# Kernel optimization log

Hardware: AMD Instinct MI355X
Metric: run time of the kernel (lower is better)

The kernel has to match this reference:

```python
import jax, jax.numpy as jnp
import numpy as np

EPS = 1e-5

def _layernorm(x, w, b):
    # x: [B, L, C]; WithBias_LayerNorm over last dim (biased variance)
    mu = jnp.mean(x, axis=-1, keepdims=True)
    var = jnp.mean((x - mu) ** 2, axis=-1, keepdims=True)
    return (x - mu) / jnp.sqrt(var + EPS) * w + b

def _selective_scan(x, x_proj_w, dt_w, A_logs, Ds):
    # x: [B, D, L]  (D = ssm d_inner = 192, N = d_state = 16, R = dt_rank = 6)
    Bsz, D, L = x.shape
    N = A_logs.shape[1]
    R = dt_w.shape[1]
    x_dbl = jnp.einsum('bdl,rd->blr', x, x_proj_w)            # [B, L, R+2N]
    dts_r = x_dbl[..., :R]
    Bs = x_dbl[..., R:R + N]                                   # [B, L, N]
    Cs = x_dbl[..., R + N:]                                    # [B, L, N]
    dts = jax.nn.softplus(jnp.einsum('blr,dr->bld', dts_r, dt_w))  # [B, L, D]
    As = -jnp.exp(A_logs.astype(jnp.float32))                  # [D, N]
    dt_A = jnp.exp(jnp.einsum('bld,dn->bldn', dts, As))        # [B, L, D, N]
    dt_B_x = jnp.einsum('bld,bln,bdl->bldn', dts, Bs, x)       # [B, L, D, N]

    def step(u, inp):
        a, bx, c = inp                                         # [B,D,N],[B,D,N],[B,N]
        u = a * u + bx
        y = jnp.einsum('bdn,bn->bd', u, c)
        return u, y

    u0 = jnp.zeros((Bsz, D, N), dtype=jnp.float32)
    _, ys = jax.lax.scan(step, u0, (jnp.swapaxes(dt_A, 0, 1),
                                     jnp.swapaxes(dt_B_x, 0, 1),
                                     jnp.swapaxes(Cs, 0, 1)))
    y = jnp.swapaxes(ys, 0, 1)                                 # [B, L, D]
    y = y + jnp.einsum('bdl,d->bld', x, Ds.astype(jnp.float32))
    return y


def setup_inputs() -> dict:
    key = jax.random.key(0)
    ks = jax.random.split(key, 12)
    B, C, H, W = 64, 2048, 24, 8
    D_in2, Dssm, N, R = 384, 192, 16, 6
    s = 0.02
    return {
        'feat_map': jax.random.normal(ks[0], (B, C, H, W), jnp.float32),
        'ln_w': jnp.ones((C,), jnp.float32),
        'ln_b': jnp.zeros((C,), jnp.float32),
        'in_w': jax.random.normal(ks[1], (D_in2, C), jnp.float32) * s,
        'in_b': jnp.zeros((D_in2,), jnp.float32),
        'x_proj_w': jax.random.normal(ks[2], (R + 2 * N, Dssm), jnp.float32) * s,
        'dt_w': jax.random.normal(ks[3], (Dssm, R), jnp.float32) * 0.1,
        'A_logs': jnp.log(jnp.broadcast_to(jnp.arange(1, N + 1, dtype=jnp.float32), (Dssm, N))),
        'Ds': jnp.ones((Dssm,), jnp.float32),
        'out_w': jax.random.normal(ks[4], (C, Dssm), jnp.float32) * s,
        'out_b': jnp.zeros((C,), jnp.float32),
        'mo_w': jax.random.normal(ks[5], (C, C), jnp.float32) * s,
        'mo_b': jnp.zeros((C,), jnp.float32),
        'bn_w': jnp.ones((C,), jnp.float32),
        'bn_b': jnp.zeros((C,), jnp.float32),
        'bn_rm': jax.random.normal(ks[6], (C,), jnp.float32) * 0.1,
        'bn_rv': jax.random.uniform(ks[7], (C,), jnp.float32) + 0.5,
    }


def reference(feat_map, ln_w, ln_b, in_w, in_b, x_proj_w, dt_w, A_logs, Ds,
              out_w, out_b, mo_w, mo_b, bn_w, bn_b, bn_rm, bn_rv):
    B, C, H, W = feat_map.shape
    L = H * W
    x3 = feat_map.transpose(0, 2, 3, 1).reshape(B, L, C)       # to_3d
    fm = _layernorm(x3, ln_w, ln_b)                            # normalized feat_map [B, L, C]
    xz = jnp.einsum('blc,oc->blo', fm, in_w) + in_b            # 1x1 conv in_proj
    x, z = jnp.split(xz, 2, axis=-1)                           # each [B, L, 192]
    xd = jnp.swapaxes(x, 1, 2)                                 # [B, D, L]
    yf = _selective_scan(xd, x_proj_w, dt_w, A_logs, Ds)       # [B, L, D]
    yb = _selective_scan(xd[:, :, ::-1], x_proj_w, dt_w, A_logs, Ds)[:, ::-1, :]
    ssm = yf + yb                                              # [B, L, D]
    ssm = ssm * jax.nn.silu(z)
    out = jnp.einsum('bld,cd->blc', ssm, out_w) + out_b        # out_proj 1x1 conv
    out = out + fm                                             # drop_path is identity at eval
    out = jnp.einsum('blc,oc->blo', out, mo_w) + mo_b          # mamba_out conv 1x1
    out = (out - bn_rm) / jnp.sqrt(bn_rv + EPS) * bn_w + bn_b  # BatchNorm (eval)
    out = jax.nn.relu(out)
    return out.reshape(B, H, W, C).transpose(0, 3, 1, 2)
```

## Files before the change

### kernel.cpp

```cpp
#include <hip/hip_runtime.h>
#include <math.h>

#define EPSV 1e-5f


typedef __attribute__((ext_vector_type(8))) __bf16 bf16x8;
typedef __attribute__((ext_vector_type(4))) float f32x4;

__device__ __forceinline__ ushort f2bf(float f) {
  union { float f; unsigned u; } v; v.f = f;
  const unsigned r = v.u + 0x7fffu + ((v.u >> 16) & 1u);
  return (ushort)(r >> 16);
}

#define GLOAD16(G, L) __builtin_amdgcn_global_load_lds( \
    (__attribute__((address_space(1))) void*)(G), \
    (__attribute__((address_space(3))) void*)(L), 16, 0, 0)

#define BAR() do { asm volatile("" ::: "memory"); \
  __builtin_amdgcn_s_barrier(); \
  asm volatile("" ::: "memory"); } while (0)

template<int CTRL>
__device__ __forceinline__ float dpp_add(float y) {
  const int s = __builtin_amdgcn_update_dpp(0, __float_as_int(y), CTRL, 0xF, 0xF, true);
  return y + __int_as_float(s);
}
__device__ __forceinline__ float reduce16(float y) {
  y = dpp_add<0xB1>(y);
  y = dpp_add<0x4E>(y);
  y = dpp_add<0x124>(y);
  y = dpp_add<0x128>(y);
  return y;
}

__global__ __launch_bounds__(256) void cvt_kernel(
    const float* __restrict__ s, ushort* __restrict__ d, int n)
{
  const int i = (blockIdx.x * 256 + threadIdx.x) * 4;
  if (i + 3 < n) {
    const float4 v = *(const float4*)(s + i);
    ushort4 o;
    o.x = f2bf(v.x); o.y = f2bf(v.y); o.z = f2bf(v.z); o.w = f2bf(v.w);
    *(ushort4*)(d + i) = o;
  }
}

__global__ __launch_bounds__(256) void transpose_w(
    const float* __restrict__ w, ushort* __restrict__ wT)
{
  __shared__ float t[64][65];
  const int c0 = blockIdx.x * 64, d0 = blockIdx.y * 64;
  const int tl = threadIdx.x & 63, tg = threadIdx.x >> 6;
#pragma unroll
  for (int r = 0; r < 16; ++r) {
    const int c = r * 4 + tg;
    t[c][tl] = w[(size_t)(c0 + c) * 192 + d0 + tl];
  }
  __syncthreads();
#pragma unroll
  for (int r = 0; r < 16; ++r) {
    const int d = r * 4 + tg;
    wT[(size_t)(d0 + d) * 2048 + c0 + tl] = f2bf(t[tl][d]);
  }
}

__global__ __launch_bounds__(256) void ln_stats(
    const float* __restrict__ feat, float* __restrict__ sums)
{
  const int b = blockIdx.x, c0 = blockIdx.y * 128;
  const int l = threadIdx.x;
  if (l >= 192) return;
  const float* p = feat + ((size_t)b * 2048 + c0) * 192 + l;
  float s = 0.f, sq = 0.f;
  for (int c = 0; c < 128; ++c) { const float v = p[(size_t)c * 192]; s += v; sq = fmaf(v, v, sq); }
  atomicAdd(&sums[(b * 192 + l) * 2], s);
  atomicAdd(&sums[(b * 192 + l) * 2 + 1], sq);
}

__global__ __launch_bounds__(256) void ln_apply(
    const float* __restrict__ feat, const float* __restrict__ sums,
    const float* __restrict__ lnw, const float* __restrict__ lnb,
    ushort* __restrict__ fm)
{
  __shared__ float tile[64][65];
  __shared__ float smu[64], srs[64];
  const int b = blockIdx.x, c0 = blockIdx.y * 64, l0 = blockIdx.z * 64;
  const int tl = threadIdx.x & 63, tg = threadIdx.x >> 6;
#pragma unroll
  for (int r = 0; r < 16; ++r) {
    const int c = r * 4 + tg;
    tile[c][tl] = feat[((size_t)b * 2048 + c0 + c) * 192 + l0 + tl];
  }
  if (threadIdx.x < 64) {
    const float s  = sums[(b * 192 + l0 + threadIdx.x) * 2];
    const float sq = sums[(b * 192 + l0 + threadIdx.x) * 2 + 1];
    const float mu = s * (1.f / 2048.f);
    smu[threadIdx.x] = mu;
    srs[threadIdx.x] = rsqrtf(sq * (1.f / 2048.f) - mu * mu + EPSV);
  }
  __syncthreads();
  const float w = lnw[c0 + tl], bb = lnb[c0 + tl];
#pragma unroll
  for (int r = 0; r < 16; ++r) {
    const int ll = r * 4 + tg;
    fm[((size_t)(b * 192 + l0 + ll)) * 2048 + c0 + tl] =
        f2bf((tile[tl][ll] - smu[ll]) * srs[ll] * w + bb);
  }
}

__device__ __forceinline__ void mfma_phase(
    const ushort* __restrict__ Ag, int lda,
    const ushort* __restrict__ Bg, int ldb, int K,
    int bm, int bn, int tid, ushort* As, ushort* Bs, f32x4 acc[4][4])
{
  const int lane = tid & 63, wave = tid >> 6;
  const int wm = (wave & 1) << 6, wn = (wave >> 1) << 6;
  const int fr = lane & 15, q = lane >> 4;
  const int r0 = tid >> 2, kc = (tid & 3) << 3;
  const int lb = (tid & 192) * 8;
  for (int k0 = 0; k0 < K; k0 += 32) {
    __syncthreads();
    GLOAD16(Ag + (size_t)(bm + r0) * lda + k0 + kc,      As + lb);
    GLOAD16(Ag + (size_t)(bm + 64 + r0) * lda + k0 + kc, As + 2048 + lb);
    GLOAD16(Bg + (size_t)(bn + r0) * ldb + k0 + kc,      Bs + lb);
    GLOAD16(Bg + (size_t)(bn + 64 + r0) * ldb + k0 + kc, Bs + 2048 + lb);
    __syncthreads();
    bf16x8 af[4], bfr[4];
#pragma unroll
    for (int i = 0; i < 4; ++i) {
      af[i]  = *(const bf16x8*)&As[(wm + i * 16 + fr) * 32 + q * 8];
      bfr[i] = *(const bf16x8*)&Bs[(wn + i * 16 + fr) * 32 + q * 8];
    }
#pragma unroll
    for (int i = 0; i < 4; ++i)
#pragma unroll
      for (int j = 0; j < 4; ++j)
        acc[i][j] = __builtin_amdgcn_mfma_f32_16x16x32_bf16(af[i], bfr[j], acc[i][j], 0, 0, 0);
  }
}

template<int MODE>
__global__ __launch_bounds__(256) void mfma_gemm(
    const ushort* __restrict__ A1, const ushort* __restrict__ B1,
    const float* __restrict__ p0,
    float* __restrict__ out, ushort* __restrict__ outb)
{
  __shared__ ushort As[4096], Bs[4096];
  const int tid = threadIdx.x;
  const int bm = blockIdx.y * 128, bn = blockIdx.x * 128;
  f32x4 acc[4][4];
#pragma unroll
  for (int i = 0; i < 4; ++i)
#pragma unroll
    for (int j = 0; j < 4; ++j) acc[i][j] = (f32x4)(0.f);

  mfma_phase(A1, 2048, B1, 2048, 2048, bm, bn, tid, As, Bs, acc);

  const int lane = tid & 63, wave = tid >> 6;
  const int wm = (wave & 1) << 6, wn = (wave >> 1) << 6;
  const int fr = lane & 15, q = lane >> 4;
  if (MODE == 0) {
#pragma unroll
    for (int mi = 0; mi < 4; ++mi) {
      const int m0 = bm + wm + mi * 16 + q * 4;
#pragma unroll
      for (int ni = 0; ni < 4; ++ni) {
        const int n = bn + wn + ni * 16 + fr;
        const float bias = p0[n];
#pragma unroll
        for (int r = 0; r < 4; ++r)
          out[(size_t)(m0 + r) * 384 + n] = acc[mi][ni][r] + bias;
      }
    }
  } else {
#pragma unroll
    for (int mi = 0; mi < 4; ++mi) {
      const int m0 = bm + wm + mi * 16 + q * 4;
#pragma unroll
      for (int ni = 0; ni < 4; ++ni) {
        const int n = bn + wn + ni * 16 + fr;
#pragma unroll
        for (int r = 0; r < 4; ++r)
          outb[(size_t)(m0 + r) * 256 + n] = f2bf(acc[mi][ni][r]);
      }
    }
  }
}

__device__ __forceinline__ void stage_half(
    int t, int kind,
    int bm, int bn, int tid,
    const ushort* __restrict__ fmw, const ushort* __restrict__ mow,
    const ushort* __restrict__ ssmb, const ushort* __restrict__ w2b,
    ushort* As, ushort* Bs)
{
  const bool isA = (kind < 2);
  const ushort* G; int ld, k0;
  if (t < 32) { G = isA ? fmw : mow;  ld = 2048; k0 = t * 64; }
  else        { G = isA ? ssmb : w2b; ld = 256;  k0 = (t - 32) * 64; }
  const int p0 = isA ? bm : bn;
  ushort* L = (isA ? As : Bs) + (t & 1) * 16384 + (kind & 1) * 8192;
  const int w = tid >> 6, l = tid & 63;
#pragma unroll
  for (int j = 0; j < 2; ++j) {
    const int LC = j * 512 + w * 64 + l;
    const int row = (kind & 1) * 128 + (LC >> 3);
    const int sc = (LC & 7) ^ (row & 7);
    GLOAD16(G + (size_t)(p0 + row) * ld + k0 + sc * 8, L + j * 4096 + w * 512);
  }
}

__global__ __launch_bounds__(512, 2) void mfma_gemm_big(
    const ushort* __restrict__ fmw,  const ushort* __restrict__ mow,
    const ushort* __restrict__ ssmb, const ushort* __restrict__ w2b,
    const float* __restrict__ scale, const float* __restrict__ shift,
    float* __restrict__ out)
{
  __shared__ ushort As[2 * 16384];
  __shared__ ushort Bs[2 * 16384];
  const int tid = threadIdx.x;
  const int flat = blockIdx.x;
  const int bx = flat & 7, by = flat >> 3;
  const int bm = by * 256, bn = bx * 256;

  const int lane = tid & 63, wave = tid >> 6;
  const int wr = wave >> 2, wc = wave & 3;
  const int fr = lane & 15, q = lane >> 4;

  constexpr int NT = 36;

  f32x4 acc[8][4];
#pragma unroll
  for (int i = 0; i < 8; ++i)
#pragma unroll
    for (int j = 0; j < 4; ++j) acc[i][j] = (f32x4)(0.f);

  stage_half(0, 0, bm, bn, tid, fmw, mow, ssmb, w2b, As, Bs);
  stage_half(0, 1, bm, bn, tid, fmw, mow, ssmb, w2b, As, Bs);
  stage_half(0, 2, bm, bn, tid, fmw, mow, ssmb, w2b, As, Bs);
  stage_half(0, 3, bm, bn, tid, fmw, mow, ssmb, w2b, As, Bs);
  stage_half(1, 2, bm, bn, tid, fmw, mow, ssmb, w2b, As, Bs);
  stage_half(1, 3, bm, bn, tid, fmw, mow, ssmb, w2b, As, Bs);
  asm volatile("s_waitcnt vmcnt(4)" ::: "memory");
  BAR();

  for (int t = 0; t < NT; ++t) {
    const ushort* Ab = As + (t & 1) * 16384;
    const ushort* Bb = Bs + (t & 1) * 16384;
    bf16x8 bfr[4];
#pragma unroll
    for (int ph = 0; ph < 4; ++ph) {
      const int ks = ph >> 1, mh = ph & 1;
      const int kswz = (((ks << 2) + q) ^ (fr & 7)) << 3;
      bf16x8 af[4];
#pragma unroll
      for (int mi = 0; mi < 4; ++mi)
        af[mi] = *(const bf16x8*)&Ab[(wr * 128 + mh * 64 + mi * 16 + fr) * 64 + kswz];
      if (mh == 0) {
#pragma unroll
        for (int ni = 0; ni < 4; ++ni)
          bfr[ni] = *(const bf16x8*)&Bb[(wc * 64 + ni * 16 + fr) * 64 + kswz];
      }
      if (ph == 0) {
        if (t + 1 < NT) stage_half(t + 1, 0, bm, bn, tid, fmw, mow, ssmb, w2b, As, Bs);
      } else if (ph == 1) {
        if (t + 1 < NT) stage_half(t + 1, 1, bm, bn, tid, fmw, mow, ssmb, w2b, As, Bs);
      } else if (ph == 3) {
        if (t + 2 < NT) {
          stage_half(t + 2, 2, bm, bn, tid, fmw, mow, ssmb, w2b, As, Bs);
          stage_half(t + 2, 3, bm, bn, tid, fmw, mow, ssmb, w2b, As, Bs);
        }
      }
      BAR();
      __builtin_amdgcn_s_setprio(1);
#pragma unroll
      for (int mi = 0; mi < 4; ++mi)
#pragma unroll
        for (int ni = 0; ni < 4; ++ni)
          acc[mh * 4 + mi][ni] = __builtin_amdgcn_mfma_f32_16x16x32_bf16(
              af[mi], bfr[ni], acc[mh * 4 + mi][ni], 0, 0, 0);
      __builtin_amdgcn_s_setprio(0);
      if (ph == 3) {
        if (t <= 33) asm volatile("s_waitcnt vmcnt(4)" ::: "memory");
        else if (t == 34) asm volatile("s_waitcnt vmcnt(0)" ::: "memory");
      }
      BAR();
    }
  }

#pragma unroll
  for (int mi = 0; mi < 8; ++mi) {
    const int m0 = bm + wr * 128 + mi * 16 + q * 4;
    const int b = m0 / 192, l0 = m0 - b * 192;
#pragma unroll
    for (int ni = 0; ni < 4; ++ni) {
      const int n = bn + wc * 64 + ni * 16 + fr;
      const float sc = scale[n], sh = shift[n];
      float4 o;
      o.x = fmaxf(fmaf(acc[mi][ni][0], sc, sh), 0.f);
      o.y = fmaxf(fmaf(acc[mi][ni][1], sc, sh), 0.f);
      o.z = fmaxf(fmaf(acc[mi][ni][2], sc, sh), 0.f);
      o.w = fmaxf(fmaf(acc[mi][ni][3], sc, sh), 0.f);
      *(float4*)(out + ((size_t)b * 2048 + n) * 192 + l0) = o;
    }
  }
}

__global__ __launch_bounds__(64) void xproj_kernel(
    const float* __restrict__ xz, const float* __restrict__ xpw,
    const float* __restrict__ dtw, float* __restrict__ dts,
    float* __restrict__ Bsb, float* __restrict__ Csb)
{
  const int m = blockIdx.x, tid = threadIdx.x;
  __shared__ float xrow[192];
  __shared__ float xdbl[38];
  const float* src = xz + (size_t)m * 384;
#pragma unroll
  for (int i = 0; i < 3; ++i) xrow[tid + i * 64] = src[tid + i * 64];
  __syncthreads();
  if (tid < 38) {
    float a = 0.f;
    const float* wr = xpw + tid * 192;
    for (int d = 0; d < 192; ++d) a = fmaf(xrow[d], wr[d], a);
    xdbl[tid] = a;
  }
  __syncthreads();
  if (tid < 16) Bsb[(size_t)m * 16 + tid] = xdbl[6 + tid];
  else if (tid < 32) Csb[(size_t)m * 16 + (tid - 16)] = xdbl[22 + (tid - 16)];
#pragma unroll
  for (int i = 0; i < 3; ++i) {
    const int d = tid + i * 64;
    const float* w = dtw + d * 6;
    float a = xdbl[0] * w[0] + xdbl[1] * w[1] + xdbl[2] * w[2]
            + xdbl[3] * w[3] + xdbl[4] * w[4] + xdbl[5] * w[5];
    dts[(size_t)m * 192 + d] = (a > 20.f) ? a : log1pf(__expf(a));
  }
}

__global__ __launch_bounds__(256) void scan_kernel(
    const float* __restrict__ xz, const float* __restrict__ dts,
    const float* __restrict__ Bsb, const float* __restrict__ Csb,
    const float* __restrict__ A_logs, const float* __restrict__ Ds,
    ushort* __restrict__ ssm)
{
  __shared__ float s_dt[16 * 196], s_x[16 * 196], s_B[16 * 196],
                   s_C[16 * 196], s_y[16 * 196];
  const int tid = threadIdx.x;
  const int b = blockIdx.x / 12, dblk = blockIdx.x - b * 12;
  const int d0 = dblk * 16;
  const size_t rbase = (size_t)b * 192;
  for (int i = tid; i < 768; i += 256) {
    const int l = i >> 2, j = (i & 3) << 2;
    const size_t row = rbase + l;
    const float4 dtv = *(const float4*)(dts + row * 192 + d0 + j);
    const float4 xv  = *(const float4*)(xz  + row * 384 + d0 + j);
    const float4 Bv  = *(const float4*)(Bsb + row * 16 + j);
    const float4 Cv  = *(const float4*)(Csb + row * 16 + j);
    s_dt[(j + 0) * 196 + l] = dtv.x; s_dt[(j + 1) * 196 + l] = dtv.y;
    s_dt[(j + 2) * 196 + l] = dtv.z; s_dt[(j + 3) * 196 + l] = dtv.w;
    s_x [(j + 0) * 196 + l] = xv.x;  s_x [(j + 1) * 196 + l] = xv.y;
    s_x [(j + 2) * 196 + l] = xv.z;  s_x [(j + 3) * 196 + l] = xv.w;
    s_B [(j + 0) * 196 + l] = Bv.x;  s_B [(j + 1) * 196 + l] = Bv.y;
    s_B [(j + 2) * 196 + l] = Bv.z;  s_B [(j + 3) * 196 + l] = Bv.w;
    s_C [(j + 0) * 196 + l] = Cv.x;  s_C [(j + 1) * 196 + l] = Cv.y;
    s_C [(j + 2) * 196 + l] = Cv.z;  s_C [(j + 3) * 196 + l] = Cv.w;
  }
  __syncthreads();
  const int n = tid & 15, dl = tid >> 4;
  const float Acoef = -expf(A_logs[(d0 + dl) * 16 + n]);
  const float* pdt = s_dt + dl * 196;
  const float* px  = s_x  + dl * 196;
  const float* pB  = s_B  + n * 196;
  const float* pC  = s_C  + n * 196;
  float* py = s_y + dl * 196;
  float u = 0.f;
  for (int l0 = 0; l0 < 192; l0 += 4) {
    const float4 dtv = *(const float4*)(pdt + l0);
    const float4 xv  = *(const float4*)(px + l0);
    const float4 Bv  = *(const float4*)(pB + l0);
    const float4 Cv  = *(const float4*)(pC + l0);
    u = fmaf(__expf(dtv.x * Acoef), u, dtv.x * Bv.x * xv.x);
    { float y = reduce16(u * Cv.x); if (n == 0) py[l0 + 0] = y; }
    u = fmaf(__expf(dtv.y * Acoef), u, dtv.y * Bv.y * xv.y);
    { float y = reduce16(u * Cv.y); if (n == 0) py[l0 + 1] = y; }
    u = fmaf(__expf(dtv.z * Acoef), u, dtv.z * Bv.z * xv.z);
    { float y = reduce16(u * Cv.z); if (n == 0) py[l0 + 2] = y; }
    u = fmaf(__expf(dtv.w * Acoef), u, dtv.w * Bv.w * xv.w);
    { float y = reduce16(u * Cv.w); if (n == 0) py[l0 + 3] = y; }
  }
  u = 0.f;
  for (int l0 = 188; l0 >= 0; l0 -= 4) {
    const float4 dtv = *(const float4*)(pdt + l0);
    const float4 xv  = *(const float4*)(px + l0);
    const float4 Bv  = *(const float4*)(pB + l0);
    const float4 Cv  = *(const float4*)(pC + l0);
    u = fmaf(__expf(dtv.w * Acoef), u, dtv.w * Bv.w * xv.w);
    { float y = reduce16(u * Cv.w); if (n == 0) py[l0 + 3] += y; }
    u = fmaf(__expf(dtv.z * Acoef), u, dtv.z * Bv.z * xv.z);
    { float y = reduce16(u * Cv.z); if (n == 0) py[l0 + 2] += y; }
    u = fmaf(__expf(dtv.y * Acoef), u, dtv.y * Bv.y * xv.y);
    { float y = reduce16(u * Cv.y); if (n == 0) py[l0 + 1] += y; }
    u = fmaf(__expf(dtv.x * Acoef), u, dtv.x * Bv.x * xv.x);
    { float y = reduce16(u * Cv.x); if (n == 0) py[l0 + 0] += y; }
  }
  __syncthreads();
  for (int i = tid; i < 768; i += 256) {
    const int l = i >> 2, j = (i & 3) << 2;
    const size_t row = rbase + l;
    float4 y4, x4;
    y4.x = s_y[(j + 0) * 196 + l]; y4.y = s_y[(j + 1) * 196 + l];
    y4.z = s_y[(j + 2) * 196 + l]; y4.w = s_y[(j + 3) * 196 + l];
    x4.x = s_x[(j + 0) * 196 + l]; x4.y = s_x[(j + 1) * 196 + l];
    x4.z = s_x[(j + 2) * 196 + l]; x4.w = s_x[(j + 3) * 196 + l];
    const float4 z4 = *(const float4*)(xz + row * 384 + 192 + d0 + j);
    const float4 D4 = *(const float4*)(Ds + d0 + j);
    ushort4 o;
    o.x = f2bf((y4.x + 2.f * x4.x * D4.x) * (z4.x / (1.f + __expf(-z4.x))));
    o.y = f2bf((y4.y + 2.f * x4.y * D4.y) * (z4.y / (1.f + __expf(-z4.y))));
    o.z = f2bf((y4.z + 2.f * x4.z * D4.z) * (z4.z / (1.f + __expf(-z4.z))));
    o.w = f2bf((y4.w + 2.f * x4.w * D4.w) * (z4.w / (1.f + __expf(-z4.w))));
    *(ushort4*)(ssm + row * 256 + d0 + j) = o;
  }
}

__global__ __launch_bounds__(64) void prep_kernel(
    const float* __restrict__ mo_w, const float* __restrict__ mo_b,
    const float* __restrict__ out_b,
    const float* __restrict__ bn_w, const float* __restrict__ bn_b,
    const float* __restrict__ bn_rm, const float* __restrict__ bn_rv,
    float* __restrict__ scale, float* __restrict__ shift)
{
  const int o = blockIdx.x, tid = threadIdx.x;
  float s = 0.f;
  for (int c = tid; c < 2048; c += 64) s = fmaf(mo_w[(size_t)o * 2048 + c], out_b[c], s);
#pragma unroll
  for (int off = 32; off > 0; off >>= 1) s += __shfl_down(s, off, 64);
  if (tid == 0) {
    const float b2 = s + mo_b[o];
    const float sc = bn_w[o] * rsqrtf(bn_rv[o] + EPSV);
    scale[o] = sc;
    shift[o] = (b2 - bn_rm[o]) * sc + bn_b[o];
  }
}

extern "C" void kernel_launch(void* const* d_in, const int* in_sizes, int n_in,
                              void* d_out, int out_size, void* d_ws, size_t ws_size,
                              hipStream_t stream) {
  const float* feat  = (const float*)d_in[0];
  const float* ln_w  = (const float*)d_in[1];
  const float* ln_b  = (const float*)d_in[2];
  const float* in_w  = (const float*)d_in[3];
  const float* in_b  = (const float*)d_in[4];
  const float* xpw   = (const float*)d_in[5];
  const float* dtw   = (const float*)d_in[6];
  const float* A_logs= (const float*)d_in[7];
  const float* Ds    = (const float*)d_in[8];
  const float* out_w = (const float*)d_in[9];
  const float* out_b = (const float*)d_in[10];
  const float* mo_w  = (const float*)d_in[11];
  const float* mo_b  = (const float*)d_in[12];
  const float* bn_w  = (const float*)d_in[13];
  const float* bn_b  = (const float*)d_in[14];
  const float* bn_rm = (const float*)d_in[15];
  const float* bn_rv = (const float*)d_in[16];
  float* out = (float*)d_out;

  uint8_t* p = (uint8_t*)d_ws;
  ushort* fm_b  = (ushort*)p; p += (size_t)12288 * 2048 * 2;
  float*  xz    = (float*)p;  p += (size_t)12288 * 384 * 4;
  float*  dts   = (float*)p;  p += (size_t)12288 * 192 * 4;
  float*  Bsb   = (float*)p;  p += (size_t)12288 * 16 * 4;
  float*  Csb   = (float*)p;  p += (size_t)12288 * 16 * 4;
  ushort* ssm_b = (ushort*)p; p += (size_t)12288 * 256 * 2;
  ushort* W2b   = (ushort*)p; p += (size_t)2048 * 256 * 2;
  ushort* owT_b = (ushort*)p; p += (size_t)256 * 2048 * 2;
  ushort* mo_wb = (ushort*)p; p += (size_t)2048 * 2048 * 2;
  ushort* in_wb = (ushort*)p; p += (size_t)384 * 2048 * 2;
  float*  scale = (float*)p;  p += 2048 * 4;
  float*  shift = (float*)p;  p += 2048 * 4;
  float*  sums  = (float*)p;  p += (size_t)64 * 192 * 2 * 4;
  if ((size_t)(p - (uint8_t*)d_ws) > ws_size) return;

  cvt_kernel<<<4096, 256, 0, stream>>>(mo_w, mo_wb, 2048 * 2048);
  cvt_kernel<<<768, 256, 0, stream>>>(in_w, in_wb, 384 * 2048);
  hipMemsetAsync(owT_b, 0, (size_t)256 * 2048 * 2, stream);
  hipMemsetAsync(ssm_b, 0, (size_t)12288 * 256 * 2, stream);
  transpose_w<<<dim3(32, 3), 256, 0, stream>>>(out_w, owT_b);

  hipMemsetAsync(sums, 0, (size_t)64 * 192 * 2 * 4, stream);
  ln_stats<<<dim3(64, 16), 256, 0, stream>>>(feat, sums);
  ln_apply<<<dim3(64, 32, 3), 256, 0, stream>>>(feat, sums, ln_w, ln_b, fm_b);

  mfma_gemm<0><<<dim3(3, 96), 256, 0, stream>>>(
      fm_b, in_wb, in_b, xz, nullptr);

  xproj_kernel<<<12288, 64, 0, stream>>>(xz, xpw, dtw, dts, Bsb, Csb);
  scan_kernel<<<768, 256, 0, stream>>>(xz, dts, Bsb, Csb, A_logs, Ds, ssm_b);

  mfma_gemm<2><<<dim3(2, 16), 256, 0, stream>>>(
      mo_wb, owT_b, nullptr, nullptr, W2b);
  prep_kernel<<<2048, 64, 0, stream>>>(mo_w, mo_b, out_b, bn_w, bn_b, bn_rm, bn_rv, scale, shift);

  mfma_gemm_big<<<384, 512, 0, stream>>>(fm_b, mo_wb, ssm_b, W2b, scale, shift, out);
}
```

Baseline: 608.7 us.

## Split-K the W2 weight-fold GEMM and merge staging phases in big GEMM

The 2048x256x2048 GEMM that folds out_proj into mamba_out weights only launched 32 blocks, leaving most CUs idle. It is now split along K into 8 slices (256 blocks) that write fp32 partials into the no-longer-needed xz buffer, followed by a reduce kernel that sums them and converts to bf16. This adds extra global traffic and a launch. Separately, the big fused GEMM now issues both halves of next-tile A staging in phase 0 instead of across phases 0 and 1, which changes load/MFMA interleaving.

```diff
diff --git a/kernel.cpp b/kernel.cpp
--- a/kernel.cpp
+++ b/kernel.cpp
@@ -140,11 +140,9 @@
   }
 }
 
-template<int MODE>
-__global__ __launch_bounds__(256) void mfma_gemm(
+__global__ __launch_bounds__(256) void mfma_gemm0(
     const ushort* __restrict__ A1, const ushort* __restrict__ B1,
-    const float* __restrict__ p0,
-    float* __restrict__ out, ushort* __restrict__ outb)
+    const float* __restrict__ p0, float* __restrict__ out)
 {
   __shared__ ushort As[4096], Bs[4096];
   const int tid = threadIdx.x;
@@ -160,32 +158,67 @@
   const int lane = tid & 63, wave = tid >> 6;
   const int wm = (wave & 1) << 6, wn = (wave >> 1) << 6;
   const int fr = lane & 15, q = lane >> 4;
-  if (MODE == 0) {
-#pragma unroll
-    for (int mi = 0; mi < 4; ++mi) {
-      const int m0 = bm + wm + mi * 16 + q * 4;
-#pragma unroll
-      for (int ni = 0; ni < 4; ++ni) {
-        const int n = bn + wn + ni * 16 + fr;
-        const float bias = p0[n];
-#pragma unroll
-        for (int r = 0; r < 4; ++r)
-          out[(size_t)(m0 + r) * 384 + n] = acc[mi][ni][r] + bias;
-      }
+#pragma unroll
+  for (int mi = 0; mi < 4; ++mi) {
+    const int m0 = bm + wm + mi * 16 + q * 4;
+#pragma unroll
+    for (int ni = 0; ni < 4; ++ni) {
+      const int n = bn + wn + ni * 16 + fr;
+      const float bias = p0[n];
+#pragma unroll
+      for (int r = 0; r < 4; ++r)
+        out[(size_t)(m0 + r) * 384 + n] = acc[mi][ni][r] + bias;
     }
-  } else {
-#pragma unroll
-    for (int mi = 0; mi < 4; ++mi) {
-      const int m0 = bm + wm + mi * 16 + q * 4;
-#pragma unroll
-      for (int ni = 0; ni < 4; ++ni) {
-        const int n = bn + wn + ni * 16 + fr;
-#pragma unroll
-        for (int r = 0; r < 4; ++r)
-          outb[(size_t)(m0 + r) * 256 + n] = f2bf(acc[mi][ni][r]);
-      }
+  }
+}
+
+__global__ __launch_bounds__(256) void w2_partial(
+    const ushort* __restrict__ A1, const ushort* __restrict__ B1,
+    float* __restrict__ part)
+{
+  __shared__ ushort As[4096], Bs[4096];
+  const int tid = threadIdx.x;
+  const int bm = blockIdx.y * 128, bn = blockIdx.x * 128;
+  const int kz = blockIdx.z * 256;
+  f32x4 acc[4][4];
+#pragma unroll
+  for (int i = 0; i < 4; ++i)
+#pragma unroll
+    for (int j = 0; j < 4; ++j) acc[i][j] = (f32x4)(0.f);
+
+  mfma_phase(A1 + kz, 2048, B1 + kz, 2048, 256, bm, bn, tid, As, Bs, acc);
+
+  const int lane = tid & 63, wave = tid >> 6;
+  const int wm = (wave & 1) << 6, wn = (wave >> 1) << 6;
+  const int fr = lane & 15, q = lane >> 4;
+  float* pout = part + (size_t)blockIdx.z * 2048 * 256;
+#pragma unroll
+  for (int mi = 0; mi < 4; ++mi) {
+    const int m0 = bm + wm + mi * 16 + q * 4;
+#pragma unroll
+    for (int ni = 0; ni < 4; ++ni) {
+      const int n = bn + wn + ni * 16 + fr;
+#pragma unroll
+      for (int r = 0; r < 4; ++r)
+        pout[(size_t)(m0 + r) * 256 + n] = acc[mi][ni][r];
     }
   }
+}
+
+__global__ __launch_bounds__(256) void w2_reduce(
+    const float* __restrict__ part, ushort* __restrict__ W2b)
+{
+  const int i = blockIdx.x * 256 + threadIdx.x;
+  const float4* p4 = (const float4*)part;
+  float4 s = p4[i];
+#pragma unroll
+  for (int z = 1; z < 8; ++z) {
+    const float4 v = p4[i + z * 131072];
+    s.x += v.x; s.y += v.y; s.z += v.z; s.w += v.w;
+  }
+  ushort4 o;
+  o.x = f2bf(s.x); o.y = f2bf(s.y); o.z = f2bf(s.z); o.w = f2bf(s.w);
+  *(ushort4*)(W2b + (size_t)i * 4) = o;
 }
 
 __device__ __forceinline__ void stage_half(
@@ -263,9 +296,10 @@
           bfr[ni] = *(const bf16x8*)&Bb[(wc * 64 + ni * 16 + fr) * 64 + kswz];
       }
       if (ph == 0) {
-        if (t + 1 < NT) stage_half(t + 1, 0, bm, bn, tid, fmw, mow, ssmb, w2b, As, Bs);
-      } else if (ph == 1) {
-        if (t + 1 < NT) stage_half(t + 1, 1, bm, bn, tid, fmw, mow, ssmb, w2b, As, Bs);
+        if (t + 1 < NT) {
+          stage_half(t + 1, 0, bm, bn, tid, fmw, mow, ssmb, w2b, As, Bs);
+          stage_half(t + 1, 1, bm, bn, tid, fmw, mow, ssmb, w2b, As, Bs);
+        }
       } else if (ph == 3) {
         if (t + 2 < NT) {
           stage_half(t + 2, 2, bm, bn, tid, fmw, mow, ssmb, w2b, As, Bs);
@@ -481,6 +515,7 @@
   float*  shift = (float*)p;  p += 2048 * 4;
   float*  sums  = (float*)p;  p += (size_t)64 * 192 * 2 * 4;
   if ((size_t)(p - (uint8_t*)d_ws) > ws_size) return;
+  float* W2part = xz;
 
   cvt_kernel<<<4096, 256, 0, stream>>>(mo_w, mo_wb, 2048 * 2048);
   cvt_kernel<<<768, 256, 0, stream>>>(in_w, in_wb, 384 * 2048);
@@ -492,14 +527,13 @@
   ln_stats<<<dim3(64, 16), 256, 0, stream>>>(feat, sums);
   ln_apply<<<dim3(64, 32, 3), 256, 0, stream>>>(feat, sums, ln_w, ln_b, fm_b);
 
-  mfma_gemm<0><<<dim3(3, 96), 256, 0, stream>>>(
-      fm_b, in_wb, in_b, xz, nullptr);
+  mfma_gemm0<<<dim3(3, 96), 256, 0, stream>>>(fm_b, in_wb, in_b, xz);
 
   xproj_kernel<<<12288, 64, 0, stream>>>(xz, xpw, dtw, dts, Bsb, Csb);
   scan_kernel<<<768, 256, 0, stream>>>(xz, dts, Bsb, Csb, A_logs, Ds, ssm_b);
 
-  mfma_gemm<2><<<dim3(2, 16), 256, 0, stream>>>(
-      mo_wb, owT_b, nullptr, nullptr, W2b);
+  w2_partial<<<dim3(2, 16, 8), 256, 0, stream>>>(mo_wb, owT_b, W2part);
+  w2_reduce<<<512, 256, 0, stream>>>(W2part, W2b);
   prep_kernel<<<2048, 64, 0, stream>>>(mo_w, mo_b, out_b, bn_w, bn_b, bn_rm, bn_rv, scale, shift);
 
   mfma_gemm_big<<<384, 512, 0, stream>>>(fm_b, mo_wb, ssm_b, W2b, scale, shift, out);
```

Measured after the change: 598.0 us. About the same (-1.8%).
